# Kernel tuning notes

Hardware: AMD Instinct MI355X
Metric: run time of the kernel (lower is better)

## Reference

```python
import jax, jax.numpy as jnp
import numpy as np

B, S, HID = 4, 2048, 2048
H, KV, D = 16, 4, 128
ROT = 32  # partial rotary dim
EPS = 1e-6
NEG = -1e9


def _rms_norm(x, w):
    # Qwen3-Next RMSNorm: fp32 norm, (1 + weight) scaling
    xf = x.astype(jnp.float32)
    out = xf * jax.lax.rsqrt(jnp.mean(xf * xf, axis=-1, keepdims=True) + EPS)
    return (out * (1.0 + w.astype(jnp.float32))).astype(x.dtype)


def _rotate_half(x):
    x1, x2 = x[..., : x.shape[-1] // 2], x[..., x.shape[-1] // 2 :]
    return jnp.concatenate((-x2, x1), axis=-1)


def setup_inputs() -> dict:
    key = jax.random.key(0)
    ks = jax.random.split(key, 8)
    hidden_states = jax.random.normal(ks[0], (B, S, HID), dtype=jnp.float32)
    # real RoPE angles for the partial rotary dims
    inv_freq = 1.0 / (10000.0 ** (np.arange(0, ROT, 2, dtype=np.float32) / ROT))
    pos = np.arange(S, dtype=np.float32)
    freqs = np.einsum('s,d->sd', pos, inv_freq)          # [S, ROT/2]
    emb = np.concatenate([freqs, freqs], axis=-1)         # [S, ROT]
    cos = jnp.broadcast_to(jnp.asarray(np.cos(emb)), (B, S, ROT))
    sin = jnp.broadcast_to(jnp.asarray(np.sin(emb)), (B, S, ROT))
    # additive causal mask [B,1,S,S]
    causal = jnp.triu(jnp.full((S, S), NEG, dtype=jnp.float32), k=1)
    attention_mask = jnp.broadcast_to(causal[None, None], (B, 1, S, S))
    std = 0.02
    wq = jax.random.normal(ks[1], (HID, H * D * 2), dtype=jnp.float32) * std
    wk = jax.random.normal(ks[2], (HID, KV * D), dtype=jnp.float32) * std
    wv = jax.random.normal(ks[3], (HID, KV * D), dtype=jnp.float32) * std
    wo = jax.random.normal(ks[4], (H * D, HID), dtype=jnp.float32) * std
    q_norm_w = jax.random.normal(ks[5], (D,), dtype=jnp.float32) * std
    k_norm_w = jax.random.normal(ks[6], (D,), dtype=jnp.float32) * std
    return {
        'hidden_states': hidden_states, 'cos': cos, 'sin': sin,
        'attention_mask': attention_mask, 'wq': wq, 'wk': wk, 'wv': wv,
        'wo': wo, 'q_norm_w': q_norm_w, 'k_norm_w': k_norm_w,
    }


def reference(hidden_states, cos, sin, attention_mask, wq, wk, wv, wo, q_norm_w, k_norm_w):
    b, s, _ = hidden_states.shape
    scaling = D ** -0.5
    # q projection -> [B,S,H,2D]; split into query and gate (chunk dim=-1)
    qg = (hidden_states @ wq).reshape(b, s, H, 2 * D)
    q, gate = qg[..., :D], qg[..., D:]
    gate = gate.reshape(b, s, H * D)
    q = _rms_norm(q, q_norm_w).transpose(0, 2, 1, 3)                    # [B,H,S,D]
    k = _rms_norm((hidden_states @ wk).reshape(b, s, KV, D), k_norm_w).transpose(0, 2, 1, 3)
    v = (hidden_states @ wv).reshape(b, s, KV, D).transpose(0, 2, 1, 3)  # [B,KV,S,D]
    # partial RoPE on first ROT dims
    c, sn = cos[:, None], sin[:, None]                                   # [B,1,S,ROT]
    q_rot, q_pass = q[..., :ROT], q[..., ROT:]
    k_rot, k_pass = k[..., :ROT], k[..., ROT:]
    q = jnp.concatenate([q_rot * c + _rotate_half(q_rot) * sn, q_pass], axis=-1)
    k = jnp.concatenate([k_rot * c + _rotate_half(k_rot) * sn, k_pass], axis=-1)
    # GQA: repeat kv heads
    groups = H // KV
    k = jnp.repeat(k, groups, axis=1)
    v = jnp.repeat(v, groups, axis=1)
    scores = jnp.einsum('bhqd,bhkd->bhqk', q, k) * scaling + attention_mask
    probs = jax.nn.softmax(scores.astype(jnp.float32), axis=-1).astype(q.dtype)
    attn = jnp.einsum('bhqk,bhkd->bhqd', probs, v)
    attn = attn.transpose(0, 2, 1, 3).reshape(b, s, H * D)
    attn = attn * jax.nn.sigmoid(gate)
    return attn @ wo
```

## Files before the change

kernel.cpp:

```cpp
#include <hip/hip_runtime.h>

#define SEQ   2048
#define NHEAD 16
#define NKV   4
#define HDIM  128
#define NB    4
#define QKVW  5120

typedef unsigned short u16;
typedef unsigned int   u32;
typedef __bf16 v8bf __attribute__((ext_vector_type(8)));
typedef float  v4f  __attribute__((ext_vector_type(4)));

__device__ __forceinline__ u16 f2bf(float f) {
  u32 u = __float_as_uint(f);
  u += 0x7fffu + ((u >> 16) & 1u);
  return (u16)(u >> 16);
}
__device__ __forceinline__ float bf2f(u16 b) {
  return __uint_as_float(((u32)b) << 16);
}

__device__ __forceinline__ void gld_lds16(const u16* g, u16* l) {
  __builtin_amdgcn_global_load_lds(
      (const __attribute__((address_space(1))) u32*)(unsigned long long)(uintptr_t)g,
      (__attribute__((address_space(3))) u32*)(u32)(uintptr_t)l,
      16, 0, 0);
}

__global__ __launch_bounds__(256) void conv_f32_bf16(const float* __restrict__ s,
                                                     u16* __restrict__ d) {
  size_t i = ((size_t)blockIdx.x * 256 + threadIdx.x) * 8;
  float4 a = *(const float4*)(s + i);
  float4 b = *(const float4*)(s + i + 4);
  uint4 o;
  o.x = (u32)f2bf(a.x) | ((u32)f2bf(a.y) << 16);
  o.y = (u32)f2bf(a.z) | ((u32)f2bf(a.w) << 16);
  o.z = (u32)f2bf(b.x) | ((u32)f2bf(b.y) << 16);
  o.w = (u32)f2bf(b.z) | ((u32)f2bf(b.w) << 16);
  *(uint4*)(d + i) = o;
}

__global__ __launch_bounds__(256) void transpose_w(const float* __restrict__ src,
                                                   u16* __restrict__ dst,
                                                   int R, int C) {
  __shared__ u16 tile[64][80];
  int t = threadIdx.x;
  int r0 = blockIdx.y * 64, c0 = blockIdx.x * 64;
  int rr = t >> 2, cc = (t & 3) * 16;
  const float* sp = src + (size_t)(r0 + rr) * C + c0 + cc;
  float4 f0 = *(const float4*)sp;
  float4 f1 = *(const float4*)(sp + 4);
  float4 f2 = *(const float4*)(sp + 8);
  float4 f3 = *(const float4*)(sp + 12);
  u16* tp = &tile[rr][cc];
  tp[0] = f2bf(f0.x);  tp[1] = f2bf(f0.y);  tp[2] = f2bf(f0.z);  tp[3] = f2bf(f0.w);
  tp[4] = f2bf(f1.x);  tp[5] = f2bf(f1.y);  tp[6] = f2bf(f1.z);  tp[7] = f2bf(f1.w);
  tp[8] = f2bf(f2.x);  tp[9] = f2bf(f2.y);  tp[10] = f2bf(f2.z); tp[11] = f2bf(f2.w);
  tp[12] = f2bf(f3.x); tp[13] = f2bf(f3.y); tp[14] = f2bf(f3.z); tp[15] = f2bf(f3.w);
  __syncthreads();
  int cr = t >> 2, rc = (t & 3) * 16;
  u32 pk[8];
#pragma unroll
  for (int i = 0; i < 8; i++) {
    u32 lo = tile[rc + 2 * i][cr];
    u32 hi = tile[rc + 2 * i + 1][cr];
    pk[i] = lo | (hi << 16);
  }
  u16* dp = dst + (size_t)(c0 + cr) * R + r0 + rc;
  uint4 o0 = {pk[0], pk[1], pk[2], pk[3]};
  uint4 o1 = {pk[4], pk[5], pk[6], pk[7]};
  *(uint4*)dp       = o0;
  *(uint4*)(dp + 8) = o1;
}

__global__ __launch_bounds__(256) void transpose_v(const u16* __restrict__ qkv,
                                                   u16* __restrict__ vt) {
  __shared__ u16 tile[64][80];
  int t = threadIdx.x;
  int s0 = blockIdx.x * 64;
  int d0 = blockIdx.y * 64;
  int bg = blockIdx.z;
  int b = bg >> 2, g = bg & 3;
  int sr = t >> 2, dc = (t & 3) * 16;
  const u16* sp = qkv + (size_t)(b * SEQ + s0 + sr) * QKVW + 4608 + g * HDIM + d0 + dc;
  *(uint4*)&tile[sr][dc]     = *(const uint4*)sp;
  *(uint4*)&tile[sr][dc + 8] = *(const uint4*)(sp + 8);
  __syncthreads();
  int dr = t >> 2, sc = (t & 3) * 16;
  u32 pk[8];
#pragma unroll
  for (int i = 0; i < 8; i++) {
    u32 lo = tile[sc + 2 * i][dr];
    u32 hi = tile[sc + 2 * i + 1][dr];
    pk[i] = lo | (hi << 16);
  }
  u16* dp = vt + ((size_t)bg * HDIM + d0 + dr) * SEQ + s0 + sc;
  uint4 o0 = {pk[0], pk[1], pk[2], pk[3]};
  uint4 o1 = {pk[4], pk[5], pk[6], pk[7]};
  *(uint4*)dp       = o0;
  *(uint4*)(dp + 8) = o1;
}

template <bool OUT_F32>
__global__ __launch_bounds__(512, 2) void gemm_bt(const u16* __restrict__ A,
                                                  const u16* __restrict__ Bt,
                                                  void* __restrict__ Cp,
                                                  int M, int N, int K) {
  __shared__ u16 As[3][256 * 32];
  __shared__ u16 Bs[3][256 * 32];
  int tid  = threadIdx.x;
  int lane = tid & 63, wave = tid >> 6;
  int wr = wave >> 2, wc = wave & 3;
  int col = lane & 15, quad = lane >> 4;
  int nwg = gridDim.x;
  int cpx = nwg >> 3;
  int id  = blockIdx.x;
  int idp = (id & 7) * cpx + (id >> 3);
  int ntile = N >> 8;
  int m0 = (idp / ntile) << 8;
  int n0 = (idp % ntile) << 8;

  v4f acc[8][4];
#pragma unroll
  for (int mi = 0; mi < 8; mi++)
#pragma unroll
    for (int ni = 0; ni < 4; ni++) acc[mi][ni] = (v4f){0.f, 0.f, 0.f, 0.f};

  int srow = tid >> 2;
  int skc  = (tid & 3) * 8;
  const u16* ag = A  + (size_t)(m0 + srow) * K + skc;
  const u16* bg = Bt + (size_t)(n0 + srow) * K + skc;
  const size_t rowK128 = (size_t)128 * K;

#define STAGE(buf, k0)                                        \
  do {                                                        \
    gld_lds16(ag + (k0),           &As[buf][tid * 8]);        \
    gld_lds16(ag + rowK128 + (k0), &As[buf][4096 + tid * 8]); \
    gld_lds16(bg + (k0),           &Bs[buf][tid * 8]);        \
    gld_lds16(bg + rowK128 + (k0), &Bs[buf][4096 + tid * 8]); \
  } while (0)

  STAGE(0, 0);
  STAGE(1, 32);
  asm volatile("s_waitcnt vmcnt(4)\n\ts_barrier" ::: "memory");

  const int NT = K >> 5;
  int cb = 0;
  for (int t = 0; t < NT; ++t) {
    int sb = cb + 2 >= 3 ? cb - 1 : cb + 2;
    if (t + 2 < NT) {
      int k0 = (t + 2) << 5;
      STAGE(sb, k0);
    }
    v8bf bfr[4];
#pragma unroll
    for (int ni = 0; ni < 4; ni++)
      bfr[ni] = *(const v8bf*)&Bs[cb][(wc * 64 + ni * 16 + col) * 32 + quad * 8];
    __builtin_amdgcn_s_setprio(1);
#pragma unroll
    for (int mi = 0; mi < 8; mi++) {
      v8bf a = *(const v8bf*)&As[cb][(wr * 128 + mi * 16 + col) * 32 + quad * 8];
#pragma unroll
      for (int ni = 0; ni < 4; ni++)
        acc[mi][ni] = __builtin_amdgcn_mfma_f32_16x16x32_bf16(a, bfr[ni], acc[mi][ni], 0, 0, 0);
    }
    __builtin_amdgcn_s_setprio(0);
    if (t < NT - 2) asm volatile("s_waitcnt vmcnt(4)\n\ts_barrier" ::: "memory");
    else            asm volatile("s_waitcnt vmcnt(0)\n\ts_barrier" ::: "memory");
    cb = cb + 1 >= 3 ? 0 : cb + 1;
  }
#undef STAGE

#pragma unroll
  for (int mi = 0; mi < 8; mi++)
#pragma unroll
    for (int ni = 0; ni < 4; ni++) {
      int r_ = m0 + wr * 128 + mi * 16 + quad * 4;
      int c_ = n0 + wc * 64 + ni * 16 + col;
#pragma unroll
      for (int r = 0; r < 4; r++) {
        if (OUT_F32) ((float*)Cp)[(size_t)(r_ + r) * N + c_] = acc[mi][ni][r];
        else         ((u16*)Cp)[(size_t)(r_ + r) * N + c_]   = f2bf(acc[mi][ni][r]);
      }
    }
}

__global__ __launch_bounds__(256) void norm_rope(u16* __restrict__ qkv,
                                                 const float* __restrict__ cosb,
                                                 const float* __restrict__ sinb,
                                                 const float* __restrict__ qw,
                                                 const float* __restrict__ kw,
                                                 u16* __restrict__ kf) {
  int wave = threadIdx.x >> 6, lane = threadIdx.x & 63;
  int tw = blockIdx.x * 4 + wave;
  int token = tw / 20, r = tw % 20;
  const u16* src;
  u16* dst;
  const float* wptr;
  if (r < 16) {
    src  = qkv + (size_t)token * QKVW + r * 256;
    dst  = (u16*)src;
    wptr = qw;
  } else {
    src  = qkv + (size_t)token * QKVW + 4096 + (r - 16) * HDIM;
    int b = token >> 11, s = token & (SEQ - 1);
    dst  = kf + ((size_t)(b * NKV + (r - 16)) * SEQ + s) * HDIM;
    wptr = kw;
  }
  int d0 = lane * 2;
  u32 x = *(const u32*)(src + d0);
  float x0 = bf2f((u16)(x & 0xffff)), x1 = bf2f((u16)(x >> 16));
  float ss = x0 * x0 + x1 * x1;
#pragma unroll
  for (int off = 1; off < 64; off <<= 1) ss += __shfl_xor(ss, off, 64);
  float sc = rsqrtf(ss * (1.f / 128.f) + 1e-6f);
  float y0 = bf2f(f2bf(x0 * sc * (1.f + wptr[d0])));
  float y1 = bf2f(f2bf(x1 * sc * (1.f + wptr[d0 + 1])));
  float p0 = __shfl_xor(y0, 8, 64);
  float p1 = __shfl_xor(y1, 8, 64);
  float z0 = y0, z1 = y1;
  if (lane < 16) {
    float c0 = cosb[(size_t)token * 32 + d0];
    float c1 = cosb[(size_t)token * 32 + d0 + 1];
    float s0 = sinb[(size_t)token * 32 + d0];
    float s1 = sinb[(size_t)token * 32 + d0 + 1];
    if (lane < 8) { z0 = y0 * c0 - p0 * s0; z1 = y1 * c1 - p1 * s1; }
    else          { z0 = y0 * c0 + p0 * s0; z1 = y1 * c1 + p1 * s1; }
  }
  u32 outp = (u32)f2bf(z0) | ((u32)f2bf(z1) << 16);
  *(u32*)(dst + d0) = outp;
}

__global__ __launch_bounds__(512) void attn_kernel(const u16* __restrict__ qkv,
                                                   const u16* __restrict__ kf,
                                                   const u16* __restrict__ vt,
                                                   u16* __restrict__ ga) {
  __shared__ u16 ks[64 * 136];
  __shared__ u16 vs[128 * 88];
  int tid = threadIdx.x, lane = tid & 63, wave = tid >> 6;
  int col = lane & 15, quad = lane >> 4;
  int qt = 15 - blockIdx.x;
  int h = blockIdx.y, b = blockIdx.z;
  int g = h >> 2;
  int qw0 = qt * 128 + wave * 16;
  int myq = qw0 + col;
  const float scl2 = 0.08838834764831845f * 1.4426950408889634f;

  v8bf qfr[4];
  const u16* qbase = qkv + (size_t)(b * SEQ + myq) * QKVW + h * 256 + quad * 8;
#pragma unroll
  for (int kc = 0; kc < 4; kc++) qfr[kc] = *(const v8bf*)(qbase + kc * 32);

  v4f o[8];
#pragma unroll
  for (int nt = 0; nt < 8; nt++) o[nt] = (v4f){0.f, 0.f, 0.f, 0.f};
  float l = 0.f;
  float m = -1e30f;

  const u16* kfb = kf + (size_t)(b * NKV + g) * SEQ * HDIM;
  const u16* vtb = vt + (size_t)(b * NKV + g) * HDIM * SEQ;

  int ksr = tid >> 4, ksd = (tid & 15) * 8;
  int vsd = tid >> 3, w8 = tid & 7;
  int voff = 32 * ((w8 >> 2) & 1) + 16 * (w8 & 1) + 4 * ((w8 >> 1) & 1);
  int vsrc = w8 * 8;

  int nk = 2 * qt + 2;
  for (int it = 0; it < nk; it++) {
    int k0 = it * 64;
    __syncthreads();
#pragma unroll
    for (int p = 0; p < 2; p++)
      *(uint4*)&ks[(p * 32 + ksr) * 136 + ksd] =
          *(const uint4*)&kfb[(size_t)(k0 + p * 32 + ksr) * HDIM + ksd];
#pragma unroll
    for (int p = 0; p < 2; p++) {
      int d = p * 64 + vsd;
      uint4 gv = *(const uint4*)&vtb[(size_t)d * SEQ + k0 + vsrc];
      uint2 w0 = {gv.x, gv.y};
      uint2 w1 = {gv.z, gv.w};
      *(uint2*)&vs[d * 88 + voff]     = w0;
      *(uint2*)&vs[d * 88 + voff + 8] = w1;
    }
    __syncthreads();

    v4f st[4];
    __builtin_amdgcn_s_setprio(1);
#pragma unroll
    for (int t = 0; t < 4; t++) {
      v4f acc = (v4f){0.f, 0.f, 0.f, 0.f};
#pragma unroll
      for (int kc = 0; kc < 4; kc++) {
        v8bf kfr = *(const v8bf*)&ks[(t * 16 + col) * 136 + kc * 32 + quad * 8];
        acc = __builtin_amdgcn_mfma_f32_16x16x32_bf16(kfr, qfr[kc], acc, 0, 0, 0);
      }
      st[t] = acc;
    }
    __builtin_amdgcn_s_setprio(0);

    bool maskw = (k0 + 63 > qw0);
    float pmax = -1e30f;
#pragma unroll
    for (int t = 0; t < 4; t++)
#pragma unroll
      for (int r = 0; r < 4; r++) {
        float x = st[t][r] * scl2;
        if (maskw && (k0 + t * 16 + quad * 4 + r > myq)) x = -1e30f;
        st[t][r] = x;
        pmax = fmaxf(pmax, x);
      }
    pmax = fmaxf(pmax, __shfl_xor(pmax, 16, 64));
    pmax = fmaxf(pmax, __shfl_xor(pmax, 32, 64));
    if (__any(pmax > m + 8.f)) {
      float nm = fmaxf(m, pmax);
      float al = exp2f(m - nm);
      m = nm;
#pragma unroll
      for (int nt = 0; nt < 8; nt++)
#pragma unroll
        for (int r = 0; r < 4; r++) o[nt][r] *= al;
      l *= al;
    }
    v8bf pb0, pb1;
    float ls = 0.f;
#pragma unroll
    for (int t = 0; t < 4; t++)
#pragma unroll
      for (int r = 0; r < 4; r++) {
        float p = exp2f(st[t][r] - m);
        ls += p;
        if (t < 2) pb0[t * 4 + r] = (__bf16)p;
        else       pb1[(t - 2) * 4 + r] = (__bf16)p;
      }
    l += ls;

    __builtin_amdgcn_s_setprio(1);
#pragma unroll
    for (int nt = 0; nt < 8; nt++) {
      v8bf vb0 = *(const v8bf*)&vs[(nt * 16 + col) * 88 + quad * 8];
      v8bf vb1 = *(const v8bf*)&vs[(nt * 16 + col) * 88 + 32 + quad * 8];
      o[nt] = __builtin_amdgcn_mfma_f32_16x16x32_bf16(vb0, pb0, o[nt], 0, 0, 0);
      o[nt] = __builtin_amdgcn_mfma_f32_16x16x32_bf16(vb1, pb1, o[nt], 0, 0, 0);
    }
    __builtin_amdgcn_s_setprio(0);
  }

  l += __shfl_xor(l, 16, 64);
  l += __shfl_xor(l, 32, 64);
  float inv = 1.f / l;
  const u16* gb = qkv + (size_t)(b * SEQ + myq) * QKVW + h * 256 + 128 + quad * 4;
  u16* ob = ga + (size_t)(b * SEQ + myq) * 2048 + h * HDIM + quad * 4;
#pragma unroll
  for (int nt = 0; nt < 8; nt++) {
    uint2 gw = *(const uint2*)(gb + nt * 16);
    float g0 = bf2f((u16)(gw.x & 0xffff)), g1 = bf2f((u16)(gw.x >> 16));
    float g2 = bf2f((u16)(gw.y & 0xffff)), g3 = bf2f((u16)(gw.y >> 16));
    float a0 = o[nt][0] * inv * (1.f / (1.f + expf(-g0)));
    float a1 = o[nt][1] * inv * (1.f / (1.f + expf(-g1)));
    float a2 = o[nt][2] * inv * (1.f / (1.f + expf(-g2)));
    float a3 = o[nt][3] * inv * (1.f / (1.f + expf(-g3)));
    uint2 ow;
    ow.x = (u32)f2bf(a0) | ((u32)f2bf(a1) << 16);
    ow.y = (u32)f2bf(a2) | ((u32)f2bf(a3) << 16);
    *(uint2*)(ob + nt * 16) = ow;
  }
}

extern "C" void kernel_launch(void* const* d_in, const int* in_sizes, int n_in,
                              void* d_out, int out_size, void* d_ws, size_t ws_size,
                              hipStream_t stream) {
  const float* hidden = (const float*)d_in[0];
  const float* cosb   = (const float*)d_in[1];
  const float* sinb   = (const float*)d_in[2];
  const float* wq  = (const float*)d_in[4];
  const float* wk  = (const float*)d_in[5];
  const float* wv  = (const float*)d_in[6];
  const float* wo  = (const float*)d_in[7];
  const float* qnw = (const float*)d_in[8];
  const float* knw = (const float*)d_in[9];
  float* out = (float*)d_out;

  u16* ws      = (u16*)d_ws;
  u16* qkv_raw = ws;
  u16* region2 = qkv_raw + (size_t)8192 * QKVW;
  u16* region3 = region2 + (size_t)8192 * 2048;
  u16* hidden_bf = region2;
  u16* g_attn    = region2;
  u16* bt_qkv    = region3;
  u16* vt        = region3;
  u16* bt_wo     = region3 + (size_t)4194304;
  u16* k_f       = region3 + (size_t)8388608;

  conv_f32_bf16<<<dim3(8192), 256, 0, stream>>>(hidden, hidden_bf);
  transpose_w<<<dim3(64, 32), 256, 0, stream>>>(wq, bt_qkv, 2048, 4096);
  transpose_w<<<dim3(8, 32), 256, 0, stream>>>(wk, bt_qkv + (size_t)4096 * 2048, 2048, 512);
  transpose_w<<<dim3(8, 32), 256, 0, stream>>>(wv, bt_qkv + (size_t)4608 * 2048, 2048, 512);
  gemm_bt<false><<<dim3(640), 512, 0, stream>>>(hidden_bf, bt_qkv, qkv_raw, 8192, QKVW, 2048);
  norm_rope<<<dim3(8192 * 20 / 4), 256, 0, stream>>>(qkv_raw, cosb, sinb, qnw, knw, k_f);
  transpose_v<<<dim3(SEQ / 64, HDIM / 64, NB * NKV), 256, 0, stream>>>(qkv_raw, vt);
  transpose_w<<<dim3(32, 32), 256, 0, stream>>>(wo, bt_wo, 2048, 2048);
  attn_kernel<<<dim3(16, NHEAD, NB), 512, 0, stream>>>(qkv_raw, k_f, vt, g_attn);
  gemm_bt<true><<<dim3(256), 512, 0, stream>>>(g_attn, bt_wo, out, 8192, 2048, 2048);
}
```

Before: 684.6 us.

## Double-buffer K/V tiles in attention with async global-to-LDS loads and XOR swizzle

The attention kernel now stages each K and V tile straight into LDS with global_load_lds, using two buffers so the next tile's load is in flight while the current tile is computed. This removes the register round-trip and one barrier per iteration. Padded LDS rows are replaced by XOR-swizzled layouts to avoid bank conflicts, and V fragments are rebuilt from four 8-byte reads. In exchange, LDS use doubles, and the swizzle and mapping must line up exactly with the MFMA operand permutation, which adds correctness risk.

```diff
diff --git a/kernel.cpp b/kernel.cpp
--- a/kernel.cpp
+++ b/kernel.cpp
@@ -26,6 +26,12 @@
       (const __attribute__((address_space(1))) u32*)(unsigned long long)(uintptr_t)g,
       (__attribute__((address_space(3))) u32*)(u32)(uintptr_t)l,
       16, 0, 0);
+}
+
+__device__ __forceinline__ v8bf mkv8(uint2 a, uint2 b) {
+  union { u32 w[4]; v8bf v; } u;
+  u.w[0] = a.x; u.w[1] = a.y; u.w[2] = b.x; u.w[3] = b.y;
+  return u.v;
 }
 
 __global__ __launch_bounds__(256) void conv_f32_bf16(const float* __restrict__ s,
@@ -236,8 +242,8 @@
                                                    const u16* __restrict__ kf,
                                                    const u16* __restrict__ vt,
                                                    u16* __restrict__ ga) {
-  __shared__ u16 ks[64 * 136];
-  __shared__ u16 vs[128 * 88];
+  __shared__ u16 ks[2][64 * 128];
+  __shared__ u16 vs[2][128 * 64];
   int tid = threadIdx.x, lane = tid & 63, wave = tid >> 6;
   int col = lane & 15, quad = lane >> 4;
   int qt = 15 - blockIdx.x;
@@ -261,29 +267,30 @@
   const u16* kfb = kf + (size_t)(b * NKV + g) * SEQ * HDIM;
   const u16* vtb = vt + (size_t)(b * NKV + g) * HDIM * SEQ;
 
-  int ksr = tid >> 4, ksd = (tid & 15) * 8;
-  int vsd = tid >> 3, w8 = tid & 7;
-  int voff = 32 * ((w8 >> 2) & 1) + 16 * (w8 & 1) + 4 * ((w8 >> 1) & 1);
-  int vsrc = w8 * 8;
+  int kRow0 = tid >> 4;
+  int kDoff = ((tid & 15) * 8) ^ (((tid >> 4) & 3) * 16);
+  const u16* kSrc0 = kfb + (size_t)kRow0 * HDIM + kDoff;
+  int vRow0 = tid >> 3;
+  int vKoff = (((tid & 7) ^ ((tid >> 3) & 7)) * 8);
+  const u16* vSrc0 = vtb + (size_t)vRow0 * SEQ + vKoff;
+
+#define ASTAGE(db, kq)                                            \
+  do {                                                            \
+    const u16* ksrc = kSrc0 + (size_t)(kq) * HDIM;                \
+    gld_lds16(ksrc,             &ks[db][tid * 8]);                \
+    gld_lds16(ksrc + 32 * HDIM, &ks[db][4096 + tid * 8]);         \
+    const u16* vsrc = vSrc0 + (kq);                               \
+    gld_lds16(vsrc,             &vs[db][tid * 8]);                \
+    gld_lds16(vsrc + 64 * SEQ,  &vs[db][4096 + tid * 8]);         \
+  } while (0)
 
   int nk = 2 * qt + 2;
+  ASTAGE(0, 0);
+  int db = 0;
   for (int it = 0; it < nk; it++) {
     int k0 = it * 64;
-    __syncthreads();
-#pragma unroll
-    for (int p = 0; p < 2; p++)
-      *(uint4*)&ks[(p * 32 + ksr) * 136 + ksd] =
-          *(const uint4*)&kfb[(size_t)(k0 + p * 32 + ksr) * HDIM + ksd];
-#pragma unroll
-    for (int p = 0; p < 2; p++) {
-      int d = p * 64 + vsd;
-      uint4 gv = *(const uint4*)&vtb[(size_t)d * SEQ + k0 + vsrc];
-      uint2 w0 = {gv.x, gv.y};
-      uint2 w1 = {gv.z, gv.w};
-      *(uint2*)&vs[d * 88 + voff]     = w0;
-      *(uint2*)&vs[d * 88 + voff + 8] = w1;
-    }
-    __syncthreads();
+    asm volatile("s_waitcnt vmcnt(0)\n\ts_barrier" ::: "memory");
+    if (it + 1 < nk) ASTAGE(db ^ 1, k0 + 64);
 
     v4f st[4];
     __builtin_amdgcn_s_setprio(1);
@@ -292,7 +299,8 @@
       v4f acc = (v4f){0.f, 0.f, 0.f, 0.f};
 #pragma unroll
       for (int kc = 0; kc < 4; kc++) {
-        v8bf kfr = *(const v8bf*)&ks[(t * 16 + col) * 136 + kc * 32 + quad * 8];
+        v8bf kfr = *(const v8bf*)&ks[db][(t * 16 + col) * 128 +
+                                         ((kc * 32 + quad * 8) ^ ((col & 3) * 16))];
         acc = __builtin_amdgcn_mfma_f32_16x16x32_bf16(kfr, qfr[kc], acc, 0, 0, 0);
       }
       st[t] = acc;
@@ -335,16 +343,24 @@
       }
     l += ls;
 
+    int sw = (col & 7) * 8;
     __builtin_amdgcn_s_setprio(1);
 #pragma unroll
     for (int nt = 0; nt < 8; nt++) {
-      v8bf vb0 = *(const v8bf*)&vs[(nt * 16 + col) * 88 + quad * 8];
-      v8bf vb1 = *(const v8bf*)&vs[(nt * 16 + col) * 88 + 32 + quad * 8];
+      int vrow = (nt * 16 + col) * 64;
+      uint2 c0 = *(const uint2*)&vs[db][vrow + ((quad * 4) ^ sw)];
+      uint2 c1 = *(const uint2*)&vs[db][vrow + ((16 + quad * 4) ^ sw)];
+      uint2 c2 = *(const uint2*)&vs[db][vrow + ((32 + quad * 4) ^ sw)];
+      uint2 c3 = *(const uint2*)&vs[db][vrow + ((48 + quad * 4) ^ sw)];
+      v8bf vb0 = mkv8(c0, c1);
+      v8bf vb1 = mkv8(c2, c3);
       o[nt] = __builtin_amdgcn_mfma_f32_16x16x32_bf16(vb0, pb0, o[nt], 0, 0, 0);
       o[nt] = __builtin_amdgcn_mfma_f32_16x16x32_bf16(vb1, pb1, o[nt], 0, 0, 0);
     }
     __builtin_amdgcn_s_setprio(0);
-  }
+    db ^= 1;
+  }
+#undef ASTAGE
 
   l += __shfl_xor(l, 16, 64);
   l += __shfl_xor(l, 32, 64);
```

New measurement: 731.8 us. 1.07x slower.
